# Kernel tuning notes

Measured on AMD Instinct MI355X. Metric: run time of the kernel, lower is better.

## Reference

```python
import jax, jax.numpy as jnp
import numpy as np

N = 50000
E = 800000
HID = 64
HEADS = 4
NUM_GRAPHS = 512
NUM_CLASSES = 120
NEG_SLOPE = 0.2


def setup_inputs() -> dict:
    key = jax.random.key(0)
    ks = jax.random.split(key, 16)
    x = jax.random.normal(ks[0], (N, HID), dtype=jnp.float32)
    edge_index = jax.random.randint(ks[1], (2, E), 0, N, dtype=jnp.int64)
    batch = jnp.sort(jax.random.randint(ks[2], (N,), 0, NUM_GRAPHS, dtype=jnp.int64))
    s = 1.0 / np.sqrt(HID)
    # GATConv layer 1: in=64, out=64, heads=4, concat=True
    W1 = jax.random.normal(ks[3], (HID, HEADS * HID), dtype=jnp.float32) * s
    a_src1 = jax.random.normal(ks[4], (HEADS, HID), dtype=jnp.float32) * s
    a_dst1 = jax.random.normal(ks[5], (HEADS, HID), dtype=jnp.float32) * s
    b1 = jnp.zeros((HEADS * HID,), dtype=jnp.float32)
    # GATConv layer 2: in=256, out=64, heads=1, concat=False
    W2 = jax.random.normal(ks[6], (HEADS * HID, HID), dtype=jnp.float32) * (1.0 / np.sqrt(HEADS * HID))
    a_src2 = jax.random.normal(ks[7], (1, HID), dtype=jnp.float32) * s
    a_dst2 = jax.random.normal(ks[8], (1, HID), dtype=jnp.float32) * s
    b2 = jnp.zeros((HID,), dtype=jnp.float32)
    # classifier
    Wc = jax.random.normal(ks[9], (HID, NUM_CLASSES), dtype=jnp.float32) * s
    bc = jnp.zeros((NUM_CLASSES,), dtype=jnp.float32)
    return {"x": x, "W1": W1, "a_src1": a_src1, "a_dst1": a_dst1, "b1": b1,
            "W2": W2, "a_src2": a_src2, "a_dst2": a_dst2, "b2": b2,
            "Wc": Wc, "bc": bc, "edge_index": edge_index, "batch": batch}


def _gat_layer(x, src, dst, W, a_src, a_dst, bias, heads, out_dim, concat):
    # x: [N, in_dim]; src/dst: [E'] (self-loops included); out per PyG GATConv (eval mode)
    n = x.shape[0]
    h = (x @ W).reshape(n, heads, out_dim)               # [N,H,D]
    al_s = jnp.einsum('nhd,hd->nh', h, a_src)             # [N,H]
    al_d = jnp.einsum('nhd,hd->nh', h, a_dst)             # [N,H]
    e = jax.nn.leaky_relu(al_s[src] + al_d[dst], NEG_SLOPE)  # [E',H]
    # segment softmax over incoming edges of each dst node
    m = jax.ops.segment_max(e, dst, num_segments=n)       # [N,H]
    e = jnp.exp(e - m[dst])
    denom = jax.ops.segment_sum(e, dst, num_segments=n)
    alpha = e / (denom[dst] + 1e-16)                      # [E',H]
    msg = h[src] * alpha[:, :, None]                      # [E',H,D]
    out = jax.ops.segment_sum(msg, dst, num_segments=n)   # [N,H,D]
    out = out.reshape(n, heads * out_dim) if concat else out.mean(axis=1)
    return out + bias


def reference(x, W1, a_src1, a_dst1, b1, W2, a_src2, a_dst2, b2, Wc, bc, edge_index, batch):
    # add self-loops (PyG GATConv default add_self_loops=True)
    loop = jnp.arange(N, dtype=edge_index.dtype)
    src = jnp.concatenate([edge_index[0], loop])
    dst = jnp.concatenate([edge_index[1], loop])
    h = _gat_layer(x, src, dst, W1, a_src1, a_dst1, b1, HEADS, HID, True)   # [N, 256]
    h = jax.nn.elu(h)
    h = _gat_layer(h, src, dst, W2, a_src2, a_dst2, b2, 1, HID, False)      # [N, 64]
    # global mean pool per graph
    sums = jax.ops.segment_sum(h, batch, num_segments=NUM_GRAPHS)           # [G, 64]
    cnt = jax.ops.segment_sum(jnp.ones((N,), dtype=h.dtype), batch, num_segments=NUM_GRAPHS)
    graph_emb = sums / jnp.maximum(cnt, 1.0)[:, None]
    return graph_emb @ Wc + bc                                              # [G, num_classes]
```

## Files before the change

kernel.cpp:

```cpp
#include <hip/hip_runtime.h>
#include <cstdint>

#define HID 64
#define HEADS 4
#define C1 256
#define NGRAPH 512
#define BCAP 5120
#define BIN_CHUNK 4096
#define LOG2E 1.44269504f

typedef unsigned short bf16_t;
typedef __attribute__((ext_vector_type(8))) short short8v;
typedef __attribute__((ext_vector_type(4))) float f32x4;

__device__ inline bf16_t f2bf(float f) {
  unsigned b = __float_as_uint(f);
  b += 0x7fffu + ((b >> 16) & 1u);
  return (bf16_t)(b >> 16);
}


__global__ __launch_bounds__(256) void const_prep(
    const float* __restrict__ W1, const float* __restrict__ a_src,
    const float* __restrict__ a_dst, const float* __restrict__ W2,
    float* __restrict__ va, bf16_t* __restrict__ W1T, bf16_t* __restrict__ W2T,
    int* __restrict__ bcnt) {
  const int idx = blockIdx.x * 256 + threadIdx.x;
  {
    const int c = idx >> 6, k = idx & 63;
    W1T[idx] = f2bf(W1[k * C1 + c]);
  }
  {
    const int c = idx >> 8, k = idx & 255;
    W2T[idx] = f2bf(W2[k * HID + c]);
  }
  if (blockIdx.x == 1) bcnt[threadIdx.x] = 0;
  if (blockIdx.x == 0) {
    const int t = threadIdx.x;
    const int h = t >> 6, k = t & 63;
    float s = 0.f, d = 0.f;
    for (int c = 0; c < 64; ++c) {
      const float w = W1[k * C1 + h * 64 + c];
      s += w * a_src[h * 64 + c];
      d += w * a_dst[h * 64 + c];
    }
    va[t] = s * LOG2E;
    va[256 + t] = d * LOG2E;
  }
}


__global__ __launch_bounds__(256) void prep_kernel(
    const float* __restrict__ x, const float* __restrict__ va,
    bf16_t* __restrict__ xbf, float4* __restrict__ als, float4* __restrict__ ald,
    int Nn) {
  const int lane = threadIdx.x & 63;
  const int g = lane >> 4, sub = lane & 15;
  const int n = (blockIdx.x * 4 + (threadIdx.x >> 6)) * 4 + g;
  if (n >= Nn) return;
  const float4 xv = *reinterpret_cast<const float4*>(x + (size_t)n * HID + 4 * sub);
  ushort4 xb;
  xb.x = f2bf(xv.x); xb.y = f2bf(xv.y); xb.z = f2bf(xv.z); xb.w = f2bf(xv.w);
  *reinterpret_cast<ushort4*>(xbf + (size_t)n * HID + 4 * sub) = xb;
  float ps[HEADS], pd[HEADS];
#pragma unroll
  for (int h = 0; h < HEADS; ++h) {
    const float4 vs = *reinterpret_cast<const float4*>(va + h * 64 + 4 * sub);
    const float4 vd = *reinterpret_cast<const float4*>(va + 256 + h * 64 + 4 * sub);
    ps[h] = xv.x * vs.x + xv.y * vs.y + xv.z * vs.z + xv.w * vs.w;
    pd[h] = xv.x * vd.x + xv.y * vd.y + xv.z * vd.z + xv.w * vd.w;
  }
#pragma unroll
  for (int off = 1; off < 16; off <<= 1) {
#pragma unroll
    for (int h = 0; h < HEADS; ++h) {
      ps[h] += __shfl_xor(ps[h], off, 16);
      pd[h] += __shfl_xor(pd[h], off, 16);
    }
  }
  if (sub == 0) {
    als[n] = make_float4(ps[0], ps[1], ps[2], ps[3]);
    ald[n] = make_float4(pd[0], pd[1], pd[2], pd[3]);
  }
}


__global__ __launch_bounds__(256) void bin_kernel(
    const int* __restrict__ ei, int* __restrict__ bcnt,
    unsigned* __restrict__ ebuf, int E, int Nn, int nbuck) {
  __shared__ unsigned ehold[BIN_CHUNK];
  __shared__ unsigned sorted[BIN_CHUNK];
  __shared__ unsigned char bkt[BIN_CHUNK];
  __shared__ unsigned char sbkt[BIN_CHUNK];
  __shared__ int hist[256], scanbuf[256], pref[256], ofs[256], gbase[256];
  const int t = threadIdx.x;
  const int base = blockIdx.x * BIN_CHUNK;
  const int total = E + Nn;
  const int m = min(BIN_CHUNK, total - base);
  if (m <= 0) return;

  hist[t] = 0;
  __syncthreads();
  for (int j = t; j < m; j += 256) {
    const int i = base + j;
    int s, d;
    if (i < E) { s = ei[i]; d = ei[E + i]; } else { s = d = i - E; }
    const int b = d >> 8;
    ehold[j] = ((unsigned)(d & 255) << 16) | (unsigned)s;
    bkt[j] = (unsigned char)b;
    atomicAdd(&hist[b], 1);
  }
  __syncthreads();
  const int v = hist[t];
  scanbuf[t] = v;
  __syncthreads();
  for (int off = 1; off < 256; off <<= 1) {
    const int p = (t >= off) ? scanbuf[t - off] : 0;
    __syncthreads();
    scanbuf[t] += p;
    __syncthreads();
  }
  pref[t] = scanbuf[t] - v;
  ofs[t] = 0;
  gbase[t] = (t < nbuck && v > 0) ? atomicAdd(&bcnt[t], v) : 0;
  __syncthreads();
  for (int j = t; j < m; j += 256) {
    const int b = bkt[j];
    const int r = atomicAdd(&ofs[b], 1);
    const int p = pref[b] + r;
    sorted[p] = ehold[j];
    sbkt[p] = (unsigned char)b;
  }
  __syncthreads();
  for (int j = t; j < m; j += 256) {
    const int b = sbkt[j];
    const int p = gbase[b] + (j - pref[b]);
    if (p < BCAP) ebuf[(size_t)b * BCAP + p] = sorted[j];
  }
}

__global__ __launch_bounds__(256) void csr_kernel(
    const int* __restrict__ bcnt, const unsigned* __restrict__ ebuf,
    int* __restrict__ csr, int* __restrict__ rowptr, int Nn, int nbuck) {
  __shared__ unsigned ent[BCAP];
  __shared__ unsigned short srt[BCAP];
  __shared__ int hist[256], scanbuf[256], pref[256], ofs[256];
  const int b = blockIdx.x, t = threadIdx.x;

  const int bv = (t < nbuck) ? min(bcnt[t], BCAP) : 0;
  scanbuf[t] = bv;
  __syncthreads();
  for (int off = 1; off < 256; off <<= 1) {
    const int p = (t >= off) ? scanbuf[t - off] : 0;
    __syncthreads();
    scanbuf[t] += p;
    __syncthreads();
  }
  const int basev = (b > 0) ? scanbuf[b - 1] : 0;
  const int totalv = scanbuf[255];
  __syncthreads();

  const int m = min(bcnt[b], BCAP);
  hist[t] = 0;
  for (int j = t; j < m; j += 256) ent[j] = ebuf[(size_t)b * BCAP + j];
  __syncthreads();
  for (int j = t; j < m; j += 256) atomicAdd(&hist[ent[j] >> 16], 1);
  __syncthreads();
  const int v = hist[t];
  scanbuf[t] = v;
  __syncthreads();
  for (int off = 1; off < 256; off <<= 1) {
    const int p = (t >= off) ? scanbuf[t - off] : 0;
    __syncthreads();
    scanbuf[t] += p;
    __syncthreads();
  }
  pref[t] = scanbuf[t] - v;
  ofs[t] = 0;
  __syncthreads();
  const int d0 = b << 8;
  const int ndst = min(256, Nn - d0);
  if (t < ndst) rowptr[d0 + t] = basev + pref[t];
  if (b == 0 && t == 0) rowptr[Nn] = totalv;
  for (int j = t; j < m; j += 256) {
    const unsigned e = ent[j];
    const int dl = (int)(e >> 16);
    const int r = atomicAdd(&ofs[dl], 1);
    srt[pref[dl] + r] = (unsigned short)(e & 0xffffu);
  }
  __syncthreads();
  for (int j = t; j < m; j += 256) csr[basev + j] = (int)srt[j];
}


__global__ __launch_bounds__(256) void msg1_agg(
    const int* __restrict__ rowptr, const int* __restrict__ csr,
    const float4* __restrict__ als4, const float4* __restrict__ ald4,
    const bf16_t* __restrict__ xbf, bf16_t* __restrict__ agg, int Nn) {
  const int wid = threadIdx.x >> 6;
  const int lane = threadIdx.x & 63;
  const int l16 = lane & 15;
  const int epar = l16 >> 3;
  const int sub8 = l16 & 7;
  int d = (blockIdx.x * 4 + wid) * 4 + (lane >> 4);
  const bool dvalid = d < Nn;
  if (!dvalid) d = Nn - 1;
  const int r0 = rowptr[d], r1 = rowptr[d + 1];
  const float4 aldv = ald4[d];

  float acc[4][8];
#pragma unroll
  for (int h = 0; h < 4; ++h)
#pragma unroll
    for (int f = 0; f < 8; ++f) acc[h][f] = 0.f;
  float ws0 = 0.f, ws1 = 0.f, ws2 = 0.f, ws3 = 0.f;

  const int base = (lane & 48) + epar;
  int cb = r0;
  int maxrem = r1 - cb;
  maxrem = max(maxrem, __shfl_xor(maxrem, 16, 64));
  maxrem = max(maxrem, __shfl_xor(maxrem, 32, 64));
  while (maxrem > 0) {
    const int eown = cb + l16;
    const int s_ = csr[min(eown, r1 - 1)];
    const float4 sv = als4[s_];
    float t0 = sv.x + aldv.x; t0 = fmaxf(t0, 0.2f * t0);
    float t1 = sv.y + aldv.y; t1 = fmaxf(t1, 0.2f * t1);
    float t2 = sv.z + aldv.z; t2 = fmaxf(t2, 0.2f * t2);
    float t3 = sv.w + aldv.w; t3 = fmaxf(t3, 0.2f * t3);
    float w0 = exp2f(t0), w1 = exp2f(t1), w2 = exp2f(t2), w3 = exp2f(t3);
    if (eown >= r1) { w0 = 0.f; w1 = 0.f; w2 = 0.f; w3 = 0.f; }
    ws0 += w0; ws1 += w1; ws2 += w2; ws3 += w3;
    const int nstep = (min(16, maxrem) + 1) >> 1;
    for (int t = 0; t < nstep; ++t) {
      const int idx = base + 2 * t;
      const float wj0 = __shfl(w0, idx, 64);
      const float wj1 = __shfl(w1, idx, 64);
      const float wj2 = __shfl(w2, idx, 64);
      const float wj3 = __shfl(w3, idx, 64);
      const int sj = __shfl(s_, idx, 64);
      const uint4 hv = *reinterpret_cast<const uint4*>(xbf + (size_t)sj * HID + 8 * sub8);
      float xv[8];
      xv[0] = __uint_as_float(hv.x << 16);
      xv[1] = __uint_as_float(hv.x & 0xffff0000u);
      xv[2] = __uint_as_float(hv.y << 16);
      xv[3] = __uint_as_float(hv.y & 0xffff0000u);
      xv[4] = __uint_as_float(hv.z << 16);
      xv[5] = __uint_as_float(hv.z & 0xffff0000u);
      xv[6] = __uint_as_float(hv.w << 16);
      xv[7] = __uint_as_float(hv.w & 0xffff0000u);
#pragma unroll
      for (int f = 0; f < 8; ++f) {
        acc[0][f] += wj0 * xv[f];
        acc[1][f] += wj1 * xv[f];
        acc[2][f] += wj2 * xv[f];
        acc[3][f] += wj3 * xv[f];
      }
    }
    cb += 16;
    maxrem = r1 - cb;
    maxrem = max(maxrem, __shfl_xor(maxrem, 16, 64));
    maxrem = max(maxrem, __shfl_xor(maxrem, 32, 64));
  }

#pragma unroll
  for (int off = 1; off < 16; off <<= 1) {
    ws0 += __shfl_xor(ws0, off, 64);
    ws1 += __shfl_xor(ws1, off, 64);
    ws2 += __shfl_xor(ws2, off, 64);
    ws3 += __shfl_xor(ws3, off, 64);
  }
#pragma unroll
  for (int h = 0; h < 4; ++h)
#pragma unroll
    for (int f = 0; f < 8; ++f) acc[h][f] += __shfl_xor(acc[h][f], 8, 64);

  if (dvalid) {
    const float i0 = 1.f / (ws0 + 1e-16f);
    const float i1 = 1.f / (ws1 + 1e-16f);
    const float i2 = 1.f / (ws2 + 1e-16f);
    const float i3 = 1.f / (ws3 + 1e-16f);
    float o0[8], o1[8];
#pragma unroll
    for (int f = 0; f < 8; ++f) {
      o0[f] = epar ? acc[2][f] : acc[0][f];
      o1[f] = epar ? acc[3][f] : acc[1][f];
    }
    const float iv0 = epar ? i2 : i0;
    const float iv1 = epar ? i3 : i1;
    const int h0 = epar * 2;
    uint4 p0, p1;
    p0.x = (unsigned)f2bf(o0[0] * iv0) | ((unsigned)f2bf(o0[1] * iv0) << 16);
    p0.y = (unsigned)f2bf(o0[2] * iv0) | ((unsigned)f2bf(o0[3] * iv0) << 16);
    p0.z = (unsigned)f2bf(o0[4] * iv0) | ((unsigned)f2bf(o0[5] * iv0) << 16);
    p0.w = (unsigned)f2bf(o0[6] * iv0) | ((unsigned)f2bf(o0[7] * iv0) << 16);
    p1.x = (unsigned)f2bf(o1[0] * iv1) | ((unsigned)f2bf(o1[1] * iv1) << 16);
    p1.y = (unsigned)f2bf(o1[2] * iv1) | ((unsigned)f2bf(o1[3] * iv1) << 16);
    p1.z = (unsigned)f2bf(o1[4] * iv1) | ((unsigned)f2bf(o1[5] * iv1) << 16);
    p1.w = (unsigned)f2bf(o1[6] * iv1) | ((unsigned)f2bf(o1[7] * iv1) << 16);
    *reinterpret_cast<uint4*>(agg + ((size_t)d * HEADS + h0) * HID + 8 * sub8) = p0;
    *reinterpret_cast<uint4*>(agg + ((size_t)d * HEADS + h0 + 1) * HID + 8 * sub8) = p1;
  }
}


__global__ __launch_bounds__(256) void gemm12_mfma(
    const bf16_t* __restrict__ agg, const bf16_t* __restrict__ W1T,
    const float* __restrict__ b1, const bf16_t* __restrict__ W2T,
    const float* __restrict__ a2s, const float* __restrict__ a2d,
    bf16_t* __restrict__ h2, float* __restrict__ als2, float* __restrict__ ald2,
    int Nn) {
  __shared__ bf16_t x2s[16][264];
  __shared__ float pbuf_s[4][16], pbuf_d[4][16];
  const int w = threadIdx.x >> 6;
  const int l = threadIdx.x & 63;
  const int n0 = blockIdx.x * 16;
  if (n0 >= Nn) return;
  const int r16 = l & 15, g = l >> 4;

  const f32x4 zz = {0.f, 0.f, 0.f, 0.f};
  f32x4 acc1[4];
#pragma unroll
  for (int ct = 0; ct < 4; ++ct) acc1[ct] = zz;

  const bf16_t* arow = agg + (size_t)(n0 + r16) * C1 + w * 64;
#pragma unroll
  for (int ks = 0; ks < 2; ++ks) {
    const short8v bfrag = *reinterpret_cast<const short8v*>(arow + ks * 32 + g * 8);
#pragma unroll
    for (int ct = 0; ct < 4; ++ct) {
      const short8v afrag = *reinterpret_cast<const short8v*>(
          W1T + (size_t)(w * 64 + ct * 16 + r16) * 64 + ks * 32 + g * 8);
      acc1[ct] = __builtin_amdgcn_mfma_f32_16x16x32_bf16(afrag, bfrag, acc1[ct], 0, 0, 0);
    }
  }

#pragma unroll
  for (int ct = 0; ct < 4; ++ct) {
    const float4 bv = *reinterpret_cast<const float4*>(b1 + w * 64 + ct * 16 + g * 4);
    float v0 = acc1[ct][0] + bv.x;
    float v1 = acc1[ct][1] + bv.y;
    float v2 = acc1[ct][2] + bv.z;
    float v3 = acc1[ct][3] + bv.w;
    v0 = v0 > 0.f ? v0 : __expf(v0) - 1.f;
    v1 = v1 > 0.f ? v1 : __expf(v1) - 1.f;
    v2 = v2 > 0.f ? v2 : __expf(v2) - 1.f;
    v3 = v3 > 0.f ? v3 : __expf(v3) - 1.f;
    uint2 pk;
    pk.x = (unsigned)f2bf(v0) | ((unsigned)f2bf(v1) << 16);
    pk.y = (unsigned)f2bf(v2) | ((unsigned)f2bf(v3) << 16);
    *reinterpret_cast<uint2*>(&x2s[r16][w * 64 + ct * 16 + g * 4]) = pk;
  }
  __syncthreads();

  f32x4 acc2 = zz;
#pragma unroll
  for (int s2 = 0; s2 < 8; ++s2) {
    const short8v bfrag = *reinterpret_cast<const short8v*>(&x2s[r16][s2 * 32 + g * 8]);
    const short8v afrag = *reinterpret_cast<const short8v*>(
        W2T + (size_t)(w * 16 + r16) * 256 + s2 * 32 + g * 8);
    acc2 = __builtin_amdgcn_mfma_f32_16x16x32_bf16(afrag, bfrag, acc2, 0, 0, 0);
  }

  const float4 avs = *reinterpret_cast<const float4*>(a2s + w * 16 + g * 4);
  const float4 avd = *reinterpret_cast<const float4*>(a2d + w * 16 + g * 4);
  float ps = acc2[0] * avs.x + acc2[1] * avs.y + acc2[2] * avs.z + acc2[3] * avs.w;
  float pd = acc2[0] * avd.x + acc2[1] * avd.y + acc2[2] * avd.z + acc2[3] * avd.w;
  ushort4 hb;
  hb.x = f2bf(acc2[0]); hb.y = f2bf(acc2[1]);
  hb.z = f2bf(acc2[2]); hb.w = f2bf(acc2[3]);
  *reinterpret_cast<ushort4*>(h2 + (size_t)(n0 + r16) * HID + w * 16 + g * 4) = hb;
  ps += __shfl_xor(ps, 16, 64);
  ps += __shfl_xor(ps, 32, 64);
  pd += __shfl_xor(pd, 16, 64);
  pd += __shfl_xor(pd, 32, 64);
  if (g == 0) { pbuf_s[w][r16] = ps; pbuf_d[w][r16] = pd; }
  __syncthreads();
  if (w == 0 && g == 0) {
    const float pst = pbuf_s[0][r16] + pbuf_s[1][r16] + pbuf_s[2][r16] + pbuf_s[3][r16];
    const float pdt = pbuf_d[0][r16] + pbuf_d[1][r16] + pbuf_d[2][r16] + pbuf_d[3][r16];
    als2[n0 + r16] = pst * LOG2E;
    ald2[n0 + r16] = pdt * LOG2E;
  }
}


__global__ __launch_bounds__(256) void msg2_fused(
    const int* __restrict__ rowptr, const int* __restrict__ csr,
    const float* __restrict__ als2, const float* __restrict__ ald2,
    const bf16_t* __restrict__ h2, const float* __restrict__ b2,
    float* __restrict__ out, int Nn) {
  const int lane = threadIdx.x & 63;
  const int g = lane >> 4, sub = lane & 15;
  const int d = (blockIdx.x * 4 + (threadIdx.x >> 6)) * 4 + g;
  if (d >= Nn) return;
  const int r0 = rowptr[d], r1 = rowptr[d + 1];
  const float aldd = ald2[d];
  float wsum = 0.f;
  float a0 = 0.f, a1 = 0.f, a2 = 0.f, a3 = 0.f;

#define M2_EDGE(EI) {                                                                \
    const int s_ = csr[EI];                                                          \
    float sc_ = als2[s_] + aldd;                                                     \
    sc_ = fmaxf(sc_, 0.2f * sc_);                                                    \
    const float w_ = exp2f(sc_);                                                     \
    wsum += w_;                                                                      \
    const uint2 hv_ = *reinterpret_cast<const uint2*>(h2 + (size_t)s_ * HID + 4 * sub); \
    a0 += w_ * __uint_as_float(hv_.x << 16);                                         \
    a1 += w_ * __uint_as_float(hv_.x & 0xffff0000u);                                 \
    a2 += w_ * __uint_as_float(hv_.y << 16);                                         \
    a3 += w_ * __uint_as_float(hv_.y & 0xffff0000u);                                 \
  }

  int e = r0;
  for (; e + 4 <= r1; e += 4) { M2_EDGE(e) M2_EDGE(e + 1) M2_EDGE(e + 2) M2_EDGE(e + 3) }
  for (; e < r1; ++e) { M2_EDGE(e) }

  const float inv = 1.f / (wsum + 1e-16f);
  const float4 bb = *reinterpret_cast<const float4*>(b2 + 4 * sub);
  float4 o;
  o.x = a0 * inv + bb.x;
  o.y = a1 * inv + bb.y;
  o.z = a2 * inv + bb.z;
  o.w = a3 * inv + bb.w;
  *reinterpret_cast<float4*>(out + (size_t)d * HID + 4 * sub) = o;
}


__device__ inline int lbound(const int* __restrict__ a, int n, int v) {
  int lo = 0, hi = n;
  while (lo < hi) { int m = (lo + hi) >> 1; if (a[m] < v) lo = m + 1; else hi = m; }
  return lo;
}

__global__ __launch_bounds__(256) void pool_cls_kernel(
    const float* __restrict__ out2, const int* __restrict__ batch,
    const float* __restrict__ Wc, const float* __restrict__ bc,
    float* __restrict__ out, int Nn, int C) {
  __shared__ float part[4][HID];
  __shared__ float es[HID];
  const int g = blockIdx.x;
  const int w = threadIdx.x >> 6;
  const int t = threadIdx.x & 63;
  const int lo = lbound(batch, Nn, g);
  const int hi = lbound(batch, Nn, g + 1);
  float acc0 = 0.f, acc1 = 0.f, acc2 = 0.f, acc3 = 0.f;
  int n = lo + w;
  for (; n + 12 < hi; n += 16) {
    acc0 += out2[(size_t)(n) * HID + t];
    acc1 += out2[(size_t)(n + 4) * HID + t];
    acc2 += out2[(size_t)(n + 8) * HID + t];
    acc3 += out2[(size_t)(n + 12) * HID + t];
  }
  for (; n < hi; n += 4) acc0 += out2[(size_t)n * HID + t];
  part[w][t] = (acc0 + acc1) + (acc2 + acc3);
  __syncthreads();
  if (w == 0) {
    const int cnt = hi - lo;
    const float cf = (float)(cnt > 1 ? cnt : 1);
    es[t] = (part[0][t] + part[1][t] + part[2][t] + part[3][t]) / cf;
  }
  __syncthreads();
  for (int c = threadIdx.x; c < C; c += 256) {
    float a = bc[c];
#pragma unroll
    for (int d = 0; d < HID; ++d) a += es[d] * Wc[d * C + c];
    out[g * C + c] = a;
  }
}

extern "C" void kernel_launch(void* const* d_in, const int* in_sizes, int n_in,
                              void* d_out, int out_size, void* d_ws, size_t ws_size,
                              hipStream_t stream) {
  const float* x      = (const float*)d_in[0];
  const float* W1     = (const float*)d_in[1];
  const float* a_src1 = (const float*)d_in[2];
  const float* a_dst1 = (const float*)d_in[3];
  const float* b1     = (const float*)d_in[4];
  const float* W2     = (const float*)d_in[5];
  const float* a_src2 = (const float*)d_in[6];
  const float* a_dst2 = (const float*)d_in[7];
  const float* b2     = (const float*)d_in[8];
  const float* Wc     = (const float*)d_in[9];
  const float* bc     = (const float*)d_in[10];
  const int*   ei     = (const int*)d_in[11];
  const int*   batch  = (const int*)d_in[12];

  const int N = in_sizes[0] / HID;
  const int E = in_sizes[11] / 2;
  const int C = in_sizes[10];
  const int Etot = E + N;
  const int nbuck = (N + 255) >> 8;

  bf16_t* AGG = (bf16_t*)d_ws;
  bf16_t* XBF = AGG + (size_t)N * C1;
  float4* ALS1 = (float4*)(XBF + (size_t)N * HID);
  float4* ALD1 = ALS1 + N;
  float* ALS2 = (float*)(ALD1 + N);
  float* ALD2 = ALS2 + N;
  int* ROWP   = (int*)(ALD2 + N);
  int* BCNT   = ROWP + (N + 4);
  int* CSR    = BCNT + 256;
  unsigned* EBUF = (unsigned*)(CSR + Etot);
  float* VA   = (float*)(EBUF + 256 * BCAP);
  bf16_t* W1T = (bf16_t*)(VA + 512);
  bf16_t* W2T = W1T + 16384;

  bf16_t* H2B = XBF;
  float* OUT2 = (float*)AGG;

  const_prep<<<64, 256, 0, stream>>>(W1, a_src1, a_dst1, W2, VA, W1T, W2T, BCNT);

  bin_kernel<<<(Etot + BIN_CHUNK - 1) / BIN_CHUNK, 256, 0, stream>>>(ei, BCNT, EBUF, E, N, nbuck);
  csr_kernel<<<nbuck, 256, 0, stream>>>(BCNT, EBUF, CSR, ROWP, N, nbuck);

  prep_kernel<<<(N + 15) / 16, 256, 0, stream>>>(x, VA, XBF, ALS1, ALD1, N);
  msg1_agg<<<(N + 15) / 16, 256, 0, stream>>>(ROWP, CSR, ALS1, ALD1, XBF, AGG, N);

  gemm12_mfma<<<(N + 15) / 16, 256, 0, stream>>>(AGG, W1T, b1, W2T, a_src2, a_dst2,
                                                 H2B, ALS2, ALD2, N);

  msg2_fused<<<(N + 15) / 16, 256, 0, stream>>>(ROWP, CSR, ALS2, ALD2, H2B, b2, OUT2, N);

  pool_cls_kernel<<<NGRAPH, 256, 0, stream>>>(OUT2, batch, Wc, bc, (float*)d_out, N, C);
}
```

Baseline: 136.7 us.

## Parallelize layer-2 edge score computation across lanes and split edges between half-groups

In the second-layer message kernel, each 16-lane group now computes attention scores for 16 edges in parallel, one per lane, instead of every lane redundantly recomputing each edge's score. Weights and source indices are broadcast by shuffle. The two 8-lane halves process alternating edges with 16-byte loads covering 8 features each, and their partial sums are combined by a cross-half shuffle reduction at the end. This removes redundant csr/als2 loads and exp2 work and widens the gather loads. The cost is extra shuffles, a wave-wide max loop bound that makes short rows idle while long rows finish, and a final reduction step.

```diff
diff --git a/kernel.cpp b/kernel.cpp
--- a/kernel.cpp
+++ b/kernel.cpp
@@ -390,40 +390,72 @@
     const float* __restrict__ als2, const float* __restrict__ ald2,
     const bf16_t* __restrict__ h2, const float* __restrict__ b2,
     float* __restrict__ out, int Nn) {
+  const int wid = threadIdx.x >> 6;
   const int lane = threadIdx.x & 63;
-  const int g = lane >> 4, sub = lane & 15;
-  const int d = (blockIdx.x * 4 + (threadIdx.x >> 6)) * 4 + g;
-  if (d >= Nn) return;
+  const int l16 = lane & 15;
+  const int epar = l16 >> 3;
+  const int sub8 = l16 & 7;
+  int d = (blockIdx.x * 4 + wid) * 4 + (lane >> 4);
+  const bool dvalid = d < Nn;
+  if (!dvalid) d = Nn - 1;
   const int r0 = rowptr[d], r1 = rowptr[d + 1];
   const float aldd = ald2[d];
-  float wsum = 0.f;
-  float a0 = 0.f, a1 = 0.f, a2 = 0.f, a3 = 0.f;
-
-#define M2_EDGE(EI) {                                                                \
-    const int s_ = csr[EI];                                                          \
-    float sc_ = als2[s_] + aldd;                                                     \
-    sc_ = fmaxf(sc_, 0.2f * sc_);                                                    \
-    const float w_ = exp2f(sc_);                                                     \
-    wsum += w_;                                                                      \
-    const uint2 hv_ = *reinterpret_cast<const uint2*>(h2 + (size_t)s_ * HID + 4 * sub); \
-    a0 += w_ * __uint_as_float(hv_.x << 16);                                         \
-    a1 += w_ * __uint_as_float(hv_.x & 0xffff0000u);                                 \
-    a2 += w_ * __uint_as_float(hv_.y << 16);                                         \
-    a3 += w_ * __uint_as_float(hv_.y & 0xffff0000u);                                 \
-  }
-
-  int e = r0;
-  for (; e + 4 <= r1; e += 4) { M2_EDGE(e) M2_EDGE(e + 1) M2_EDGE(e + 2) M2_EDGE(e + 3) }
-  for (; e < r1; ++e) { M2_EDGE(e) }
-
-  const float inv = 1.f / (wsum + 1e-16f);
-  const float4 bb = *reinterpret_cast<const float4*>(b2 + 4 * sub);
-  float4 o;
-  o.x = a0 * inv + bb.x;
-  o.y = a1 * inv + bb.y;
-  o.z = a2 * inv + bb.z;
-  o.w = a3 * inv + bb.w;
-  *reinterpret_cast<float4*>(out + (size_t)d * HID + 4 * sub) = o;
+
+  float acc[8];
+#pragma unroll
+  for (int f = 0; f < 8; ++f) acc[f] = 0.f;
+  float ws = 0.f;
+
+  const int base = (lane & 48) + epar;
+  int cb = r0;
+  int maxrem = r1 - cb;
+  maxrem = max(maxrem, __shfl_xor(maxrem, 16, 64));
+  maxrem = max(maxrem, __shfl_xor(maxrem, 32, 64));
+  while (maxrem > 0) {
+    const int eown = cb + l16;
+    const int s_ = csr[min(eown, r1 - 1)];
+    float sc = als2[s_] + aldd;
+    sc = fmaxf(sc, 0.2f * sc);
+    float w = exp2f(sc);
+    if (eown >= r1) w = 0.f;
+    ws += w;
+    const int nstep = (min(16, maxrem) + 1) >> 1;
+    for (int t = 0; t < nstep; ++t) {
+      const int idx = base + 2 * t;
+      const float wj = __shfl(w, idx, 64);
+      const int sj = __shfl(s_, idx, 64);
+      const uint4 hv = *reinterpret_cast<const uint4*>(h2 + (size_t)sj * HID + 8 * sub8);
+      acc[0] += wj * __uint_as_float(hv.x << 16);
+      acc[1] += wj * __uint_as_float(hv.x & 0xffff0000u);
+      acc[2] += wj * __uint_as_float(hv.y << 16);
+      acc[3] += wj * __uint_as_float(hv.y & 0xffff0000u);
+      acc[4] += wj * __uint_as_float(hv.z << 16);
+      acc[5] += wj * __uint_as_float(hv.z & 0xffff0000u);
+      acc[6] += wj * __uint_as_float(hv.w << 16);
+      acc[7] += wj * __uint_as_float(hv.w & 0xffff0000u);
+    }
+    cb += 16;
+    maxrem = r1 - cb;
+    maxrem = max(maxrem, __shfl_xor(maxrem, 16, 64));
+    maxrem = max(maxrem, __shfl_xor(maxrem, 32, 64));
+  }
+
+#pragma unroll
+  for (int off = 1; off < 16; off <<= 1) ws += __shfl_xor(ws, off, 64);
+#pragma unroll
+  for (int f = 0; f < 8; ++f) acc[f] += __shfl_xor(acc[f], 8, 64);
+
+  if (dvalid) {
+    const float inv = 1.f / (ws + 1e-16f);
+    const int fo = 8 * sub8 + 4 * epar;
+    const float4 bb = *reinterpret_cast<const float4*>(b2 + fo);
+    float4 o;
+    o.x = (epar ? acc[4] : acc[0]) * inv + bb.x;
+    o.y = (epar ? acc[5] : acc[1]) * inv + bb.y;
+    o.z = (epar ? acc[6] : acc[2]) * inv + bb.z;
+    o.w = (epar ? acc[7] : acc[3]) * inv + bb.w;
+    *reinterpret_cast<float4*>(out + (size_t)d * HID + fo) = o;
+  }
 }
 
 
```

After: 135.7 us. Within noise of the previous version (-0.7%).
